# Kernel optimization log

Hardware: AMD Instinct MI355X
Metric: run time of the kernel (lower is better)

The kernel has to match this reference:

```python
import jax, jax.numpy as jnp
import numpy as np

N_SOURCE = 100000
N_TARGET = 4096
DEG = 800                      # edges per target (uniform)
N_EDGES = N_TARGET * DEG       # 3,276,800
SOURCE_DIM = 512
EMBED_DIM = 32
TARGET_DIM = 16


def setup_inputs() -> dict:
    key = jax.random.key(0)
    k1, k2, k3, k4, k5 = jax.random.split(key, 5)
    source_feat = jax.random.normal(k1, (N_SOURCE, SOURCE_DIM), dtype=jnp.float32)
    embed = jax.random.normal(k2, (SOURCE_DIM, EMBED_DIM), dtype=jnp.float32)
    weight = jax.random.normal(k3, (EMBED_DIM, TARGET_DIM), dtype=jnp.float32)
    # edges sorted by target; range_list[i] = [start, end) of target i's edge block
    src = jax.random.randint(k4, (N_EDGES,), 0, N_SOURCE, dtype=jnp.int64)
    tgt = jnp.repeat(jnp.arange(N_TARGET, dtype=jnp.int64), DEG)
    edge_index = jnp.stack([src, tgt], axis=0)
    starts = jnp.arange(N_TARGET, dtype=jnp.int64) * DEG
    range_list = jnp.stack([starts, starts + DEG], axis=1)
    x_norm = jax.random.uniform(k5, (N_SOURCE,), dtype=jnp.float32) + 0.5
    return {"source_feat": source_feat, "embed": embed, "weight": weight,
            "edge_index": edge_index, "range_list": range_list, "x_norm": x_norm}


def reference(source_feat, embed, weight, edge_index, range_list, x_norm):
    # dense embed GEMM + row normalization
    x = jnp.matmul(source_feat, embed)              # [N_SOURCE, EMBED_DIM]
    x = x / x_norm[:, None]
    # hierarchical conv: gather source rows, mean-aggregate per target segment
    tmp = x[edge_index[0]]                           # [N_EDGES, EMBED_DIM]
    agg = jax.ops.segment_sum(tmp, edge_index[1], num_segments=N_TARGET)
    deg = (range_list[:, 1] - range_list[:, 0]).astype(x.dtype)
    out = agg / jnp.maximum(deg, 1.0)[:, None]       # [N_TARGET, EMBED_DIM]
    out = jnp.matmul(out, weight)                    # [N_TARGET, TARGET_DIM]
    return out
```

## Files before the change

kernel.cpp:

```cpp
#include <hip/hip_runtime.h>
#include <hip/hip_bf16.h>

#define N_SOURCE   100000
#define N_TARGET   4096
#define SOURCE_DIM 512
#define EMBED_DIM  32
#define TARGET_DIM 16
#define NTILES     (N_SOURCE / 16)
#define TILES_PER_WAVE 2

typedef __attribute__((ext_vector_type(8))) short short8;
typedef __attribute__((ext_vector_type(4))) float f32x4;

static __device__ __forceinline__ ushort f2bf(float f) {
    __hip_bfloat16 h = __float2bfloat16(f);
    return *(ushort*)&h;
}

__global__ __launch_bounds__(256)
void k_embed_weight(const float* __restrict__ embed,
                    const float* __restrict__ weight,
                    ushort* __restrict__ Mt) {
    __shared__ float wlds[EMBED_DIM * TARGET_DIM];
    int tid = threadIdx.x;
    for (int i = tid; i < EMBED_DIM * TARGET_DIM; i += 256)
        wlds[i] = weight[i];
    __syncthreads();

    int idx = blockIdx.x * 256 + tid;
    if (idx < SOURCE_DIM * TARGET_DIM) {
        int k = idx >> 4;
        int o = idx & 15;
        float s = 0.f;
        #pragma unroll
        for (int j = 0; j < EMBED_DIM; ++j)
            s += embed[k * EMBED_DIM + j] * wlds[j * TARGET_DIM + o];
        Mt[o * SOURCE_DIM + k] = f2bf(s);
    }
}

__global__ __launch_bounds__(256, 2)
void k_gemm_y(const float*  __restrict__ A,
              const float*  __restrict__ xnorm,
              const ushort* __restrict__ Mt,
              ushort*       __restrict__ y) {
    int tid  = threadIdx.x;
    int wave = tid >> 6;
    int lane = tid & 63;
    int n    = lane & 15;
    int g    = lane >> 4;

    short8 bfrag[16];
    #pragma unroll
    for (int kk = 0; kk < 16; ++kk)
        bfrag[kk] = *(const short8*)(Mt + n * SOURCE_DIM + kk * 32 + g * 8);

    int tbase = blockIdx.x * (4 * TILES_PER_WAVE) + wave * TILES_PER_WAVE;

    #pragma unroll
    for (int t = 0; t < TILES_PER_WAVE; ++t) {
        int tile = tbase + t;
        if (tile >= NTILES) break;
        int row0 = tile * 16;
        const float* Arow = A + (size_t)(row0 + n) * SOURCE_DIM + g * 8;

        f32x4 acc = {0.f, 0.f, 0.f, 0.f};
        #pragma unroll
        for (int kk = 0; kk < 16; ++kk) {
            float4 a0 = *(const float4*)(Arow + kk * 32);
            float4 a1 = *(const float4*)(Arow + kk * 32 + 4);
            short8 af;
            af[0] = (short)f2bf(a0.x); af[1] = (short)f2bf(a0.y);
            af[2] = (short)f2bf(a0.z); af[3] = (short)f2bf(a0.w);
            af[4] = (short)f2bf(a1.x); af[5] = (short)f2bf(a1.y);
            af[6] = (short)f2bf(a1.z); af[7] = (short)f2bf(a1.w);
            acc = __builtin_amdgcn_mfma_f32_16x16x32_bf16(af, bfrag[kk], acc, 0, 0, 0);
        }

        int m0 = g * 4;
        float4 xn = *(const float4*)(xnorm + row0 + m0);
        const float xr[4] = {xn.x, xn.y, xn.z, xn.w};
        #pragma unroll
        for (int r = 0; r < 4; ++r)
            y[(size_t)(row0 + m0 + r) * TARGET_DIM + n] = f2bf(acc[r] / xr[r]);
    }
}

__global__ __launch_bounds__(256)
void k_gather_mean(const ushort* __restrict__ y,
                   const int*    __restrict__ src,
                   const int*    __restrict__ rl,
                   float* __restrict__ out) {
    int t     = blockIdx.x;
    int tid   = threadIdx.x;
    int start = rl[2 * t];
    int end   = rl[2 * t + 1];

    int slot = tid >> 1;
    int sub  = tid & 1;

    float a[8];
    #pragma unroll
    for (int i = 0; i < 8; ++i) a[i] = 0.f;

    for (int base = start + slot * 4; base < end; base += 512) {
        int rem = end - base;
        int id[4];
        if (rem >= 4) {
            int4 q = *(const int4*)(src + base);
            id[0] = q.x; id[1] = q.y; id[2] = q.z; id[3] = q.w;
        } else {
            #pragma unroll
            for (int j = 0; j < 4; ++j) id[j] = (j < rem) ? src[base + j] : 0;
        }
        #pragma unroll
        for (int j = 0; j < 4; ++j) {
            if (j < rem) {
                uint4 v = *(const uint4*)(y + (size_t)id[j] * TARGET_DIM + sub * 8);
                const uint w[4] = {v.x, v.y, v.z, v.w};
                #pragma unroll
                for (int i = 0; i < 4; ++i) {
                    uint lo = w[i] << 16;
                    uint hi = w[i] & 0xffff0000u;
                    a[2 * i]     += *(float*)&lo;
                    a[2 * i + 1] += *(float*)&hi;
                }
            }
        }
    }

    #pragma unroll
    for (int m = 2; m <= 32; m <<= 1) {
        #pragma unroll
        for (int i = 0; i < 8; ++i) a[i] += __shfl_xor(a[i], m);
    }

    __shared__ float red[4][16];
    int wid  = tid >> 6;
    int lane = tid & 63;
    if (lane < 2) {
        #pragma unroll
        for (int i = 0; i < 8; ++i) red[wid][lane * 8 + i] = a[i];
    }
    __syncthreads();

    if (tid < TARGET_DIM) {
        float s = red[0][tid] + red[1][tid] + red[2][tid] + red[3][tid];
        float deg = (float)(end - start);
        deg = deg > 1.f ? deg : 1.f;
        out[t * TARGET_DIM + tid] = s / deg;
    }
}

extern "C" void kernel_launch(void* const* d_in, const int* in_sizes, int n_in,
                              void* d_out, int out_size, void* d_ws, size_t ws_size,
                              hipStream_t stream) {
    const float* source_feat = (const float*)d_in[0];
    const float* embed       = (const float*)d_in[1];
    const float* weight      = (const float*)d_in[2];
    const int*   edge_src    = (const int*)d_in[3];
    const int*   range_list  = (const int*)d_in[4];
    const float* x_norm      = (const float*)d_in[5];

    float*  out = (float*)d_out;
    ushort* Mt  = (ushort*)d_ws;
    ushort* y   = (ushort*)((char*)d_ws + 16384);

    k_embed_weight<<<32, 256, 0, stream>>>(embed, weight, Mt);

    int nblk = (NTILES + 4 * TILES_PER_WAVE - 1) / (4 * TILES_PER_WAVE);
    k_gemm_y<<<nblk, 256, 0, stream>>>(source_feat, x_norm, Mt, y);

    k_gather_mean<<<N_TARGET, 256, 0, stream>>>(y, edge_src, range_list, out);
}
```

Before: 71.67 us.

## Stage B fragments in LDS and use one tile per wave with higher occupancy

The projected weight matrix now goes into shared memory once per block, and each MFMA step reads its B fragment from LDS. Previously all 16 fragments were held in registers per lane. Each wave now handles a single 16-row tile, the grid is twice as large, and launch bounds are raised to 4 blocks per CU. The goal is to cut VGPR pressure so more waves can be in flight to hide the memory latency of streaming the 200MB source feature matrix. The cost is an LDS fill and barrier in every block plus more total block launches.

```diff
diff --git a/kernel.cpp b/kernel.cpp
--- a/kernel.cpp
+++ b/kernel.cpp
@@ -6,8 +6,7 @@
 #define SOURCE_DIM 512
 #define EMBED_DIM  32
 #define TARGET_DIM 16
-#define NTILES     (N_SOURCE / 16)
-#define TILES_PER_WAVE 2
+#define NTILES     ((N_SOURCE + 15) / 16)
 
 typedef __attribute__((ext_vector_type(8))) short short8;
 typedef __attribute__((ext_vector_type(4))) float f32x4;
@@ -39,42 +38,48 @@
     }
 }
 
-__global__ __launch_bounds__(256, 2)
+__global__ __launch_bounds__(256, 4)
 void k_gemm_y(const float*  __restrict__ A,
               const float*  __restrict__ xnorm,
               const ushort* __restrict__ Mt,
               ushort*       __restrict__ y) {
+    __shared__ ushort Bl[SOURCE_DIM * TARGET_DIM];
     int tid  = threadIdx.x;
     int wave = tid >> 6;
     int lane = tid & 63;
     int n    = lane & 15;
     int g    = lane >> 4;
 
-    short8 bfrag[16];
     #pragma unroll
-    for (int kk = 0; kk < 16; ++kk)
-        bfrag[kk] = *(const short8*)(Mt + n * SOURCE_DIM + kk * 32 + g * 8);
+    for (int i = 0; i < 4; ++i) {
+        int c  = tid + 256 * i;
+        int nn = c & 15;
+        int kg = c >> 4;
+        int kk = kg >> 2;
+        int gg = kg & 3;
+        *(uint4*)&Bl[c * 8] =
+            *(const uint4*)(Mt + nn * SOURCE_DIM + kk * 32 + gg * 8);
+    }
+    __syncthreads();
 
-    int tbase = blockIdx.x * (4 * TILES_PER_WAVE) + wave * TILES_PER_WAVE;
-
-    #pragma unroll
-    for (int t = 0; t < TILES_PER_WAVE; ++t) {
-        int tile = tbase + t;
-        if (tile >= NTILES) break;
+    int tile = blockIdx.x * 4 + wave;
+    if (tile < NTILES) {
         int row0 = tile * 16;
         const float* Arow = A + (size_t)(row0 + n) * SOURCE_DIM + g * 8;
+        const ushort* Bll = Bl + lane * 8;
 
         f32x4 acc = {0.f, 0.f, 0.f, 0.f};
         #pragma unroll
         for (int kk = 0; kk < 16; ++kk) {
             float4 a0 = *(const float4*)(Arow + kk * 32);
             float4 a1 = *(const float4*)(Arow + kk * 32 + 4);
+            short8 bf = *(const short8*)(Bll + kk * 512);
             short8 af;
             af[0] = (short)f2bf(a0.x); af[1] = (short)f2bf(a0.y);
             af[2] = (short)f2bf(a0.z); af[3] = (short)f2bf(a0.w);
             af[4] = (short)f2bf(a1.x); af[5] = (short)f2bf(a1.y);
             af[6] = (short)f2bf(a1.z); af[7] = (short)f2bf(a1.w);
-            acc = __builtin_amdgcn_mfma_f32_16x16x32_bf16(af, bfrag[kk], acc, 0, 0, 0);
+            acc = __builtin_amdgcn_mfma_f32_16x16x32_bf16(af, bf, acc, 0, 0, 0);
         }
 
         int m0 = g * 4;
@@ -168,7 +173,7 @@
 
     k_embed_weight<<<32, 256, 0, stream>>>(embed, weight, Mt);
 
-    int nblk = (NTILES + 4 * TILES_PER_WAVE - 1) / (4 * TILES_PER_WAVE);
+    int nblk = (NTILES + 3) / 4;
     k_gemm_y<<<nblk, 256, 0, stream>>>(source_feat, x_norm, Mt, y);
 
     k_gather_mean<<<N_TARGET, 256, 0, stream>>>(y, edge_src, range_list, out);
```

Result: faster. 67.74 us (-5.5%).
